# Performance work log

Measured on AMD Instinct MI355X. Metric: run time of the kernel, lower is better.

Reference implementation:

```python
import jax, jax.numpy as jnp
import numpy as np
import math

B, N, M, O = 64, 2048, 64, 128  # batch, neurons, in_dims, out_dims


def setup_inputs() -> dict:
    key = jax.random.key(0)
    kx, kw, kb = jax.random.split(key, 3)
    s = 1.0 / math.sqrt(M + O)
    x = jax.random.normal(kx, (B, N, M), dtype=jnp.float32)
    # master weights fp32, init U(-s, s) as in the torch module
    w1 = jax.random.uniform(kw, (M, O, N), dtype=jnp.float32, minval=-s, maxval=s)
    b1 = jnp.zeros((1, N, O), dtype=jnp.float32)
    return {"x": x, "w1": w1, "b1": b1}


def reference(x, w1, b1):
    # N independent per-neuron linears: [B,N,M] x [M,O,N] -> [B,N,O]
    # cast master weights/bias to compute dtype (matches .to(x.dtype))
    w = w1.astype(x.dtype)
    b = b1.astype(x.dtype)
    return jnp.einsum('bnm,mon->bno', x, w) + b
```

## Files before the change

### kernel.cpp

```cpp
#include <hip/hip_runtime.h>
#include <hip/hip_bf16.h>

#define N_TOT 2048
#define M_DIM 64
#define O_DIM 128
#define NT 8

typedef __bf16 bf16x8 __attribute__((ext_vector_type(8)));
typedef __bf16 bf16x4 __attribute__((ext_vector_type(4)));
typedef float f32x4 __attribute__((ext_vector_type(4)));

__global__ __launch_bounds__(512, 2) void superlinear_mfma(
    const float* __restrict__ x, const float* __restrict__ w1,
    const float* __restrict__ b1, float* __restrict__ out)
{
    __shared__ unsigned char wlds[2 * NT * 16 * M_DIM * 2];

    const int tid  = threadIdx.x;
    const int lane = tid & 63;
    const int wave = tid >> 6;

    const int bid  = blockIdx.x;
    const int nblk = (bid & 7) * 32 + (bid >> 3);
    const int n0   = nblk * NT;
    const int n    = n0 + wave;

    const int col = lane & 15;
    const int kg  = lane >> 4;

    const int half = tid & 1;
    const int ol   = (tid >> 1) & 15;
    const int m4   = (tid >> 5) * 4;

    const size_t MSTR = (size_t)O_DIM * N_TOT;

    auto stage_issue = [&](int ot, float4* r) {
        const float* gp = w1 + (size_t)m4 * MSTR + (size_t)(ot * 16 + ol) * N_TOT
                             + n0 + half * 4;
        r[0] = *(const float4*)gp;
        r[1] = *(const float4*)(gp + MSTR);
        r[2] = *(const float4*)(gp + 2 * MSTR);
        r[3] = *(const float4*)(gp + 3 * MSTR);
    };
    auto stage_write = [&](int ot, const float4* r) {
        unsigned base = (unsigned)(ot & 1) << 14;
        const float* a0 = (const float*)&r[0];
        const float* a1 = (const float*)&r[1];
        const float* a2 = (const float*)&r[2];
        const float* a3 = (const float*)&r[3];
        #pragma unroll
        for (int j = 0; j < 4; ++j) {
            int nn = half * 4 + j;
            bf16x4 pk;
            pk[0] = (__bf16)a0[j];
            pk[1] = (__bf16)a1[j];
            pk[2] = (__bf16)a2[j];
            pk[3] = (__bf16)a3[j];
            unsigned addr = (unsigned)(nn * 2048 + ol * 128 + m4 * 2);
            addr ^= (unsigned)((ol & 7) << 4);
            *(bf16x4*)(wlds + base + addr) = pk;
        }
    };

    float4 sr[4];
    stage_issue(0, sr);

    float bv[8];
    #pragma unroll
    for (int ot = 0; ot < 8; ++ot)
        bv[ot] = b1[(size_t)n * O_DIM + ot * 16 + col];

    float4 xr[2][4][2];
    #pragma unroll
    for (int kc = 0; kc < 2; ++kc)
        #pragma unroll
        for (int bt = 0; bt < 4; ++bt) {
            int b = bt * 16 + col;
            const float* xp = x + ((size_t)b * N_TOT + n) * M_DIM + kc * 32 + kg * 8;
            xr[kc][bt][0] = *(const float4*)xp;
            xr[kc][bt][1] = *(const float4*)(xp + 4);
        }

    stage_write(0, sr);

    bf16x8 af[2][4];
    #pragma unroll
    for (int kc = 0; kc < 2; ++kc)
        #pragma unroll
        for (int bt = 0; bt < 4; ++bt) {
            const float* lp = (const float*)&xr[kc][bt][0];
            const float* hp = (const float*)&xr[kc][bt][1];
            bf16x8 v;
            #pragma unroll
            for (int j = 0; j < 4; ++j) {
                v[j]     = (__bf16)lp[j];
                v[4 + j] = (__bf16)hp[j];
            }
            af[kc][bt] = v;
        }

    asm volatile("s_waitcnt lgkmcnt(0)" ::: "memory");
    __builtin_amdgcn_s_barrier();
    __builtin_amdgcn_sched_barrier(0);

    #pragma unroll
    for (int ot = 0; ot < 8; ++ot) {
        float4 srn[4];
        if (ot < 7) stage_issue(ot + 1, srn);

        unsigned base = (unsigned)(ot & 1) << 14;
        unsigned addr = (unsigned)(wave * 2048 + col * 128 + kg * 16);
        addr ^= (unsigned)((col & 7) << 4);
        bf16x8 bf0 = *(const bf16x8*)(wlds + base + addr);
        bf16x8 bf1 = *(const bf16x8*)(wlds + base + (addr ^ 64u));

        f32x4 a[4];
        #pragma unroll
        for (int bt = 0; bt < 4; ++bt) {
            f32x4 ci;
            ci[0] = bv[ot]; ci[1] = bv[ot]; ci[2] = bv[ot]; ci[3] = bv[ot];
            a[bt] = __builtin_amdgcn_mfma_f32_16x16x32_bf16(af[0][bt], bf0, ci,    0, 0, 0);
            a[bt] = __builtin_amdgcn_mfma_f32_16x16x32_bf16(af[1][bt], bf1, a[bt], 0, 0, 0);
        }

        if (ot < 7) stage_write(ot + 1, srn);

        #pragma unroll
        for (int bt = 0; bt < 4; ++bt)
            #pragma unroll
            for (int r = 0; r < 4; ++r) {
                int b = bt * 16 + kg * 4 + r;
                out[((size_t)b * N_TOT + n) * O_DIM + ot * 16 + col] = a[bt][r];
            }

        if (ot < 7) {
            asm volatile("s_waitcnt lgkmcnt(0)" ::: "memory");
            __builtin_amdgcn_s_barrier();
            __builtin_amdgcn_sched_barrier(0);
        }
    }
}

extern "C" void kernel_launch(void* const* d_in, const int* in_sizes, int n_in,
                              void* d_out, int out_size, void* d_ws, size_t ws_size,
                              hipStream_t stream) {
    const float* x  = (const float*)d_in[0];
    const float* w1 = (const float*)d_in[1];
    const float* b1 = (const float*)d_in[2];
    float* out = (float*)d_out;
    superlinear_mfma<<<dim3(256), dim3(512), 0, stream>>>(x, w1, b1, out);
}
```

Before: 35.70 us.

## Stage weights in 32-column chunks with triple-buffered LDS and two-deep prefetch

Result: no change. 35.42 us (median of 2 runs) (-0.8%).

```diff
diff --git a/kernel.cpp b/kernel.cpp
--- a/kernel.cpp
+++ b/kernel.cpp
@@ -7,14 +7,13 @@
 #define NT 8
 
 typedef __bf16 bf16x8 __attribute__((ext_vector_type(8)));
-typedef __bf16 bf16x4 __attribute__((ext_vector_type(4)));
 typedef float f32x4 __attribute__((ext_vector_type(4)));
 
 __global__ __launch_bounds__(512, 2) void superlinear_mfma(
     const float* __restrict__ x, const float* __restrict__ w1,
     const float* __restrict__ b1, float* __restrict__ out)
 {
-    __shared__ unsigned char wlds[2 * NT * 16 * M_DIM * 2];
+    __shared__ unsigned char wlds[3 * NT * 32 * M_DIM * 2];
 
     const int tid  = threadIdx.x;
     const int lane = tid & 63;
@@ -29,46 +28,35 @@
     const int kg  = lane >> 4;
 
     const int half = tid & 1;
-    const int ol   = (tid >> 1) & 15;
-    const int m4   = (tid >> 5) * 4;
+    const int ol   = (tid >> 1) & 31;
+    const int mseg = tid >> 6;
 
     const size_t MSTR = (size_t)O_DIM * N_TOT;
 
-    auto stage_issue = [&](int ot, float4* r) {
-        const float* gp = w1 + (size_t)m4 * MSTR + (size_t)(ot * 16 + ol) * N_TOT
+    auto stage_issue = [&](int c, float4* r) {
+        const float* gp = w1 + ((size_t)(mseg * 8) * O_DIM + (c * 32 + ol)) * N_TOT
                              + n0 + half * 4;
-        r[0] = *(const float4*)gp;
-        r[1] = *(const float4*)(gp + MSTR);
-        r[2] = *(const float4*)(gp + 2 * MSTR);
-        r[3] = *(const float4*)(gp + 3 * MSTR);
+        #pragma unroll
+        for (int mm = 0; mm < 8; ++mm)
+            r[mm] = *(const float4*)(gp + (size_t)mm * MSTR);
     };
-    auto stage_write = [&](int ot, const float4* r) {
-        unsigned base = (unsigned)(ot & 1) << 14;
-        const float* a0 = (const float*)&r[0];
-        const float* a1 = (const float*)&r[1];
-        const float* a2 = (const float*)&r[2];
-        const float* a3 = (const float*)&r[3];
+    auto stage_write = [&](int c, const float4* r) {
+        unsigned base = (unsigned)(c % 3) * 32768u;
         #pragma unroll
         for (int j = 0; j < 4; ++j) {
             int nn = half * 4 + j;
-            bf16x4 pk;
-            pk[0] = (__bf16)a0[j];
-            pk[1] = (__bf16)a1[j];
-            pk[2] = (__bf16)a2[j];
-            pk[3] = (__bf16)a3[j];
-            unsigned addr = (unsigned)(nn * 2048 + ol * 128 + m4 * 2);
+            bf16x8 v;
+            #pragma unroll
+            for (int mm = 0; mm < 8; ++mm)
+                v[mm] = (__bf16)(((const float*)&r[mm])[j]);
+            unsigned addr = (unsigned)(nn * 4096 + ol * 128 + mseg * 16);
             addr ^= (unsigned)((ol & 7) << 4);
-            *(bf16x4*)(wlds + base + addr) = pk;
+            *(bf16x8*)(wlds + base + addr) = v;
         }
     };
 
-    float4 sr[4];
-    stage_issue(0, sr);
-
-    float bv[8];
-    #pragma unroll
-    for (int ot = 0; ot < 8; ++ot)
-        bv[ot] = b1[(size_t)n * O_DIM + ot * 16 + col];
+    float4 srA[8], srB[8];
+    stage_issue(0, srA);
 
     float4 xr[2][4][2];
     #pragma unroll
@@ -80,8 +68,14 @@
             xr[kc][bt][0] = *(const float4*)xp;
             xr[kc][bt][1] = *(const float4*)(xp + 4);
         }
+    float bv[8];
+    #pragma unroll
+    for (int ot = 0; ot < 8; ++ot)
+        bv[ot] = b1[(size_t)n * O_DIM + ot * 16 + col];
 
-    stage_write(0, sr);
+    stage_issue(1, srB);
+
+    stage_write(0, srA);
 
     bf16x8 af[2][4];
     #pragma unroll
@@ -103,37 +97,41 @@
     __builtin_amdgcn_s_barrier();
     __builtin_amdgcn_sched_barrier(0);
 
+    const unsigned sw = (unsigned)(col & 7) << 4;
     #pragma unroll
-    for (int ot = 0; ot < 8; ++ot) {
-        float4 srn[4];
-        if (ot < 7) stage_issue(ot + 1, srn);
+    for (int c = 0; c < 4; ++c) {
+        if (c < 2) stage_issue(c + 2, (c & 1) ? srB : srA);
 
-        unsigned base = (unsigned)(ot & 1) << 14;
-        unsigned addr = (unsigned)(wave * 2048 + col * 128 + kg * 16);
-        addr ^= (unsigned)((col & 7) << 4);
-        bf16x8 bf0 = *(const bf16x8*)(wlds + base + addr);
-        bf16x8 bf1 = *(const bf16x8*)(wlds + base + (addr ^ 64u));
-
-        f32x4 a[4];
+        unsigned base = (unsigned)(c % 3) * 32768u;
+        f32x4 acc[4][2];
         #pragma unroll
-        for (int bt = 0; bt < 4; ++bt) {
+        for (int otl = 0; otl < 2; ++otl) {
+            unsigned la = (unsigned)(wave * 4096 + otl * 2048 + col * 128 + kg * 16);
+            bf16x8 bf0 = *(const bf16x8*)(wlds + base + (la ^ sw));
+            bf16x8 bf1 = *(const bf16x8*)(wlds + base + ((la + 64) ^ sw));
             f32x4 ci;
-            ci[0] = bv[ot]; ci[1] = bv[ot]; ci[2] = bv[ot]; ci[3] = bv[ot];
-            a[bt] = __builtin_amdgcn_mfma_f32_16x16x32_bf16(af[0][bt], bf0, ci,    0, 0, 0);
-            a[bt] = __builtin_amdgcn_mfma_f32_16x16x32_bf16(af[1][bt], bf1, a[bt], 0, 0, 0);
+            float b0 = bv[c * 2 + otl];
+            ci[0] = b0; ci[1] = b0; ci[2] = b0; ci[3] = b0;
+            #pragma unroll
+            for (int bt = 0; bt < 4; ++bt) {
+                acc[bt][otl] = __builtin_amdgcn_mfma_f32_16x16x32_bf16(af[0][bt], bf0, ci,           0, 0, 0);
+                acc[bt][otl] = __builtin_amdgcn_mfma_f32_16x16x32_bf16(af[1][bt], bf1, acc[bt][otl], 0, 0, 0);
+            }
         }
 
-        if (ot < 7) stage_write(ot + 1, srn);
+        if (c < 3) stage_write(c + 1, (c & 1) ? srA : srB);
 
         #pragma unroll
         for (int bt = 0; bt < 4; ++bt)
             #pragma unroll
             for (int r = 0; r < 4; ++r) {
                 int b = bt * 16 + kg * 4 + r;
-                out[((size_t)b * N_TOT + n) * O_DIM + ot * 16 + col] = a[bt][r];
+                float* op = out + ((size_t)b * N_TOT + n) * O_DIM + c * 32 + col;
+                op[0]  = acc[bt][0][r];
+                op[16] = acc[bt][1][r];
             }
 
-        if (ot < 7) {
+        if (c < 3) {
             asm volatile("s_waitcnt lgkmcnt(0)" ::: "memory");
             __builtin_amdgcn_s_barrier();
             __builtin_amdgcn_sched_barrier(0);
```
